# Kernel tuning notes

Hardware: AMD Instinct MI355X
Metric: run time of the kernel (lower is better)

The kernel has to match this reference:

```python
import jax, jax.numpy as jnp
import numpy as np
from jax import lax

REP_THR = 0.6
BORDER = 10


def setup_inputs() -> dict:
    key = jax.random.key(0)
    # repeatability heatmap in [0, 1), NCHW
    repeatability = jax.random.uniform(key, (16, 1, 1536, 1536), dtype=jnp.float32)
    return {"repeatability": repeatability}


def _local_max(x):
    # 3x3 stride-1 max pool with padding=1 (torch pads with -inf for maxpool)
    return lax.reduce_window(
        x, -jnp.inf, lax.max,
        window_dimensions=(1, 1, 3, 3),
        window_strides=(1, 1, 1, 1),
        padding=((0, 0), (0, 0), (1, 1), (1, 1)),
    )


def reference(repeatability):
    B, C, H, W = repeatability.shape
    maxima = (repeatability == _local_max(repeatability)) & (repeatability >= REP_THR)
    # border mask: zero out a 10-pixel frame
    border = jnp.zeros((H, W), dtype=bool).at[BORDER:-BORDER, BORDER:-BORDER].set(True)
    maxima = maxima & border  # broadcasts over (B, C)
    # nonzero().t()[2:4] -> row/col (y, x) coordinates of surviving maxima, shape [2, K]
    idx = jnp.nonzero(maxima)  # tuple (b, c, y, x); dynamic-shaped, eager only
    return jnp.stack(idx)[2:4]
```

## Files before the change

### kernel.cpp

```cpp
#include <hip/hip_runtime.h>

#define W 1536
#define H 1536
#define NB 16
#define NROWS (NB * H)
#define SH 32
#define NBLK1 (NROWS / SH)
#define BLOCK1 384
#define RING 8
#define CPR 24
#define NMASK (NROWS * CPR)
#define REP_THR 0.6f

__device__ __forceinline__ float max3f(float a, float b, float c) {
    return fmaxf(fmaxf(a, b), c);
}

__global__ __launch_bounds__(BLOCK1) void nms_pass1(const float* __restrict__ in,
                                                    unsigned long long* __restrict__ masks,
                                                    unsigned int* __restrict__ counts) {
    __shared__ float smem[RING * W];
    __shared__ unsigned wsum[BLOCK1 / 64];
    const int t = threadIdx.x;
    const int lane = t & 63;
    const int wv = t >> 6;
    const int blk = blockIdx.x;
    const int img = blk / 48;
    const int ytile = blk - img * 48;
    const int R0 = img * H + ytile * SH;
    const int rlo = R0 - 1;

    auto issue_step = [&](int s) {
        const int rel0 = 4 * s;
#pragma unroll
        for (int j = 0; j < 4; ++j) {
            int ir = rlo + rel0 + j;
            ir = ir < 0 ? 0 : (ir >= NROWS ? NROWS - 1 : ir);
            const float* g = in + (size_t)ir * W + 4 * t;
            float* l = smem + ((rel0 + j) & (RING - 1)) * W + (wv << 8);
            __builtin_amdgcn_global_load_lds(
                (const __attribute__((address_space(1))) unsigned int*)g,
                (__attribute__((address_space(3))) unsigned int*)l, 16, 0, 0);
        }
    };

    const int cl = (t == 0) ? 0 : (4 * t - 4);
    const int cr = (t == BLOCK1 - 1) ? 4 * t : (4 * t + 4);
    auto read_row = [&](int rel, float* r) {
        const float* base = smem + (rel & (RING - 1)) * W;
        float4 L = *(const float4*)(base + cl);
        float4 C = *(const float4*)(base + 4 * t);
        float4 R = *(const float4*)(base + cr);
        r[0] = L.w; r[1] = C.x; r[2] = C.y; r[3] = C.z; r[4] = C.w; r[5] = R.x;
    };

    unsigned colm = 0xFu;
    if (4 * t + 3 < 10) colm = 0u;
    else if (4 * t < 10) colm = 0xCu;
    if (4 * t > 1525) colm = 0u;
    else if (4 * t + 3 > 1525) colm &= 0x3u;

    issue_step(0);
    issue_step(1);

    float rA[6], rB[6], rC[6];
    unsigned cnt = 0;

#pragma unroll 1
    for (int s = 1; s <= SH / 4; ++s) {
        __syncthreads();
        if (s == 1) { read_row(0, rA); read_row(1, rB); }
        const int yb = ytile * SH + 4 * (s - 1);
#pragma unroll
        for (int r = 0; r < 4; ++r) {
            read_row(4 * (s - 1) + 2 + r, rC);
            const int y = yb + r;
            unsigned nib = 0u;
            if (y >= 10 && y < H - 10) {
                float cm0 = max3f(rA[0], rB[0], rC[0]);
                float cm1 = max3f(rA[1], rB[1], rC[1]);
                float cm2 = max3f(rA[2], rB[2], rC[2]);
                float cm3 = max3f(rA[3], rB[3], rC[3]);
                float cm4 = max3f(rA[4], rB[4], rC[4]);
                float cm5 = max3f(rA[5], rB[5], rC[5]);
                nib |= (rB[1] >= fmaxf(max3f(cm0, cm1, cm2), REP_THR)) ? 1u : 0u;
                nib |= (rB[2] >= fmaxf(max3f(cm1, cm2, cm3), REP_THR)) ? 2u : 0u;
                nib |= (rB[3] >= fmaxf(max3f(cm2, cm3, cm4), REP_THR)) ? 4u : 0u;
                nib |= (rB[4] >= fmaxf(max3f(cm3, cm4, cm5), REP_THR)) ? 8u : 0u;
                nib &= colm;
            }
#pragma unroll
            for (int k = 0; k < 6; ++k) { rA[k] = rB[k]; rB[k] = rC[k]; }
            cnt += __popc(nib);
            unsigned x = nib;
            x |= __shfl_down(x, 1, 64) << 4;
            x |= __shfl_down(x, 2, 64) << 8;
            x |= __shfl_down(x, 4, 64) << 16;
            unsigned hi = __shfl_down(x, 8, 64);
            if ((lane & 15) == 0) {
                unsigned long long m64 = (unsigned long long)x | ((unsigned long long)hi << 32);
                masks[(size_t)(img * H + y) * CPR + (t >> 4)] = m64;
            }
        }
        __syncthreads();
        if (s < SH / 4) issue_step(s + 1);
    }

#pragma unroll
    for (int o = 32; o > 0; o >>= 1) cnt += __shfl_down(cnt, o, 64);
    if (lane == 0) wsum[wv] = cnt;
    __syncthreads();
    if (t == 0) {
        unsigned sum = 0;
#pragma unroll
        for (int k = 0; k < BLOCK1 / 64; ++k) sum += wsum[k];
        counts[blk] = sum;
    }
}

__global__ __launch_bounds__(256) void nms_scan(const unsigned int* __restrict__ counts,
                                                unsigned int* __restrict__ offsets) {
    const int t = threadIdx.x;
    const int lane = t & 63, wv = t >> 6;
    unsigned v0 = counts[3 * t], v1 = counts[3 * t + 1], v2 = counts[3 * t + 2];
    unsigned sum = v0 + v1 + v2;
    unsigned incl = sum;
#pragma unroll
    for (int o = 1; o < 64; o <<= 1) {
        unsigned u = __shfl_up(incl, o, 64);
        if (lane >= o) incl += u;
    }
    __shared__ unsigned wtot[4];
    if (lane == 63) wtot[wv] = incl;
    __syncthreads();
    unsigned base = incl - sum;
#pragma unroll
    for (int k = 0; k < 4; ++k) base += (k < wv) ? wtot[k] : 0u;
    offsets[3 * t] = base;
    offsets[3 * t + 1] = base + v0;
    offsets[3 * t + 2] = base + v0 + v1;
}

__global__ __launch_bounds__(256) void nms_pass3(const unsigned long long* __restrict__ masks,
                                                 const unsigned int* __restrict__ offsets,
                                                 int* __restrict__ out, unsigned int K) {
    const int t = threadIdx.x, lane = t & 63, wv = t >> 6;
    const int blk = blockIdx.x;
    unsigned long long m[3];
    unsigned cnt = 0;
#pragma unroll
    for (int k = 0; k < 3; ++k) {
        m[k] = masks[(size_t)blk * (SH * CPR) + 3 * t + k];
        cnt += (unsigned)__popcll(m[k]);
    }
    unsigned incl = cnt;
#pragma unroll
    for (int o = 1; o < 64; o <<= 1) {
        unsigned u = __shfl_up(incl, o, 64);
        if (lane >= o) incl += u;
    }
    __shared__ unsigned wtot[4];
    if (lane == 63) wtot[wv] = incl;
    __syncthreads();
    unsigned wbase = 0;
#pragma unroll
    for (int k = 0; k < 4; ++k) wbase += (k < wv) ? wtot[k] : 0u;
    unsigned pos = offsets[blk] + wbase + (incl - cnt);
    const int ybase = (blk % 48) * SH;
#pragma unroll
    for (int k = 0; k < 3; ++k) {
        unsigned long long mm = m[k];
        if (mm) {
            const int q = 3 * t + k;
            const int y = ybase + q / CPR;
            const int x0 = (q % CPR) * 64;
            while (mm) {
                int j = __builtin_ctzll(mm);
                mm &= mm - 1ull;
                if (pos < K) { out[pos] = y; out[K + pos] = x0 + j; }
                ++pos;
            }
        }
    }
}

extern "C" void kernel_launch(void* const* d_in, const int* in_sizes, int n_in,
                              void* d_out, int out_size, void* d_ws, size_t ws_size,
                              hipStream_t stream) {
    const float* in = (const float*)d_in[0];
    int* out = (int*)d_out;
    unsigned long long* masks = (unsigned long long*)d_ws;
    unsigned int* counts = (unsigned int*)((char*)d_ws + (size_t)NMASK * 8);
    unsigned int* offsets = counts + NBLK1;
    const unsigned K = (unsigned)(out_size / 2);

    nms_pass1<<<NBLK1, BLOCK1, 0, stream>>>(in, masks, counts);
    nms_scan<<<1, 256, 0, stream>>>(counts, offsets);
    nms_pass3<<<NBLK1, 256, 0, stream>>>(masks, offsets, out, K);
}
```

Measured before the change: 267.2 us.

## Replace LDS ring staging with direct register loads and separable max

Drops the global_load_lds ring buffer and barriers in pass1. Each thread instead loads two overlapping unaligned float4s per row straight into registers, computes the horizontal 3-max once per row, and reuses it across the vertical window. The row tile is halved to 16 so there are twice as many blocks, and the scan and compaction kernels are resized to match. The aim is to remove LDS traffic and sync stalls, at the cost of unaligned and partly redundant global loads and more, shorter blocks.

```diff
diff --git a/kernel.cpp b/kernel.cpp
--- a/kernel.cpp
+++ b/kernel.cpp
@@ -4,10 +4,9 @@
 #define H 1536
 #define NB 16
 #define NROWS (NB * H)
-#define SH 32
+#define SH 16
 #define NBLK1 (NROWS / SH)
 #define BLOCK1 384
-#define RING 8
 #define CPR 24
 #define NMASK (NROWS * CPR)
 #define REP_THR 0.6f
@@ -16,105 +15,97 @@
     return fmaxf(fmaxf(a, b), c);
 }
 
+__device__ __forceinline__ float4 ld4u(const float* p) {
+    float4 r;
+    __builtin_memcpy(&r, p, 16);
+    return r;
+}
+
 __global__ __launch_bounds__(BLOCK1) void nms_pass1(const float* __restrict__ in,
                                                     unsigned long long* __restrict__ masks,
                                                     unsigned int* __restrict__ counts) {
-    __shared__ float smem[RING * W];
-    __shared__ unsigned wsum[BLOCK1 / 64];
     const int t = threadIdx.x;
     const int lane = t & 63;
     const int wv = t >> 6;
     const int blk = blockIdx.x;
-    const int img = blk / 48;
-    const int ytile = blk - img * 48;
-    const int R0 = img * H + ytile * SH;
-    const int rlo = R0 - 1;
+    const int r0 = blk * SH;
+    const int ytile = blk % (H / SH);
 
-    auto issue_step = [&](int s) {
-        const int rel0 = 4 * s;
-#pragma unroll
-        for (int j = 0; j < 4; ++j) {
-            int ir = rlo + rel0 + j;
-            ir = ir < 0 ? 0 : (ir >= NROWS ? NROWS - 1 : ir);
-            const float* g = in + (size_t)ir * W + 4 * t;
-            float* l = smem + ((rel0 + j) & (RING - 1)) * W + (wv << 8);
-            __builtin_amdgcn_global_load_lds(
-                (const __attribute__((address_space(1))) unsigned int*)g,
-                (__attribute__((address_space(3))) unsigned int*)l, 16, 0, 0);
-        }
+    const int ca = (t == 0) ? 0 : 4 * t - 1;
+    const int cb = (t == BLOCK1 - 1) ? 4 * t : 4 * t + 1;
+
+    unsigned colm = 0xFu;
+    if (t <= 1) colm = 0u;
+    else if (t == 2) colm = 0xCu;
+    if (t >= 382) colm = 0u;
+    else if (t == 381) colm = 0x3u;
+
+    auto rowp = [&](int i) {
+        int ir = r0 - 1 + i;
+        ir = ir < 0 ? 0 : (ir >= NROWS ? NROWS - 1 : ir);
+        return in + (size_t)ir * W;
     };
 
-    const int cl = (t == 0) ? 0 : (4 * t - 4);
-    const int cr = (t == BLOCK1 - 1) ? 4 * t : (4 * t + 4);
-    auto read_row = [&](int rel, float* r) {
-        const float* base = smem + (rel & (RING - 1)) * W;
-        float4 L = *(const float4*)(base + cl);
-        float4 C = *(const float4*)(base + 4 * t);
-        float4 R = *(const float4*)(base + cr);
-        r[0] = L.w; r[1] = C.x; r[2] = C.y; r[3] = C.z; r[4] = C.w; r[5] = R.x;
-    };
+    float4 va0 = ld4u(rowp(0) + ca), vb0 = ld4u(rowp(0) + cb);
+    float4 va1 = ld4u(rowp(1) + ca), vb1 = ld4u(rowp(1) + cb);
+    float4 vaN = ld4u(rowp(2) + ca), vbN = ld4u(rowp(2) + cb);
 
-    unsigned colm = 0xFu;
-    if (4 * t + 3 < 10) colm = 0u;
-    else if (4 * t < 10) colm = 0xCu;
-    if (4 * t > 1525) colm = 0u;
-    else if (4 * t + 3 > 1525) colm &= 0x3u;
+    float4 hA, hB, ctrB;
+    hA.x = max3f(va0.x, va0.y, va0.z);
+    hA.y = max3f(va0.y, va0.z, va0.w);
+    hA.z = max3f(vb0.x, vb0.y, vb0.z);
+    hA.w = max3f(vb0.y, vb0.z, vb0.w);
+    hB.x = max3f(va1.x, va1.y, va1.z);
+    hB.y = max3f(va1.y, va1.z, va1.w);
+    hB.z = max3f(vb1.x, vb1.y, vb1.z);
+    hB.w = max3f(vb1.y, vb1.z, vb1.w);
+    ctrB.x = va1.y; ctrB.y = va1.z; ctrB.z = va1.w; ctrB.w = vb1.z;
 
-    issue_step(0);
-    issue_step(1);
+    unsigned cnt = 0;
+#pragma unroll
+    for (int i = 2; i <= SH + 1; ++i) {
+        float4 va = vaN, vb = vbN;
+        vaN = ld4u(rowp(i + 1) + ca);
+        vbN = ld4u(rowp(i + 1) + cb);
+        float4 hC;
+        hC.x = max3f(va.x, va.y, va.z);
+        hC.y = max3f(va.y, va.z, va.w);
+        hC.z = max3f(vb.x, vb.y, vb.z);
+        hC.w = max3f(vb.y, vb.z, vb.w);
 
-    float rA[6], rB[6], rC[6];
-    unsigned cnt = 0;
-
-#pragma unroll 1
-    for (int s = 1; s <= SH / 4; ++s) {
-        __syncthreads();
-        if (s == 1) { read_row(0, rA); read_row(1, rB); }
-        const int yb = ytile * SH + 4 * (s - 1);
-#pragma unroll
-        for (int r = 0; r < 4; ++r) {
-            read_row(4 * (s - 1) + 2 + r, rC);
-            const int y = yb + r;
-            unsigned nib = 0u;
-            if (y >= 10 && y < H - 10) {
-                float cm0 = max3f(rA[0], rB[0], rC[0]);
-                float cm1 = max3f(rA[1], rB[1], rC[1]);
-                float cm2 = max3f(rA[2], rB[2], rC[2]);
-                float cm3 = max3f(rA[3], rB[3], rC[3]);
-                float cm4 = max3f(rA[4], rB[4], rC[4]);
-                float cm5 = max3f(rA[5], rB[5], rC[5]);
-                nib |= (rB[1] >= fmaxf(max3f(cm0, cm1, cm2), REP_THR)) ? 1u : 0u;
-                nib |= (rB[2] >= fmaxf(max3f(cm1, cm2, cm3), REP_THR)) ? 2u : 0u;
-                nib |= (rB[3] >= fmaxf(max3f(cm2, cm3, cm4), REP_THR)) ? 4u : 0u;
-                nib |= (rB[4] >= fmaxf(max3f(cm3, cm4, cm5), REP_THR)) ? 8u : 0u;
-                nib &= colm;
-            }
-#pragma unroll
-            for (int k = 0; k < 6; ++k) { rA[k] = rB[k]; rB[k] = rC[k]; }
-            cnt += __popc(nib);
-            unsigned x = nib;
-            x |= __shfl_down(x, 1, 64) << 4;
-            x |= __shfl_down(x, 2, 64) << 8;
-            x |= __shfl_down(x, 4, 64) << 16;
-            unsigned hi = __shfl_down(x, 8, 64);
-            if ((lane & 15) == 0) {
-                unsigned long long m64 = (unsigned long long)x | ((unsigned long long)hi << 32);
-                masks[(size_t)(img * H + y) * CPR + (t >> 4)] = m64;
-            }
+        const int yloc = ytile * SH + (i - 2);
+        unsigned nib = 0u;
+        if (yloc >= 10 && yloc < H - 10) {
+            nib |= (ctrB.x >= fmaxf(max3f(hA.x, hB.x, hC.x), REP_THR)) ? 1u : 0u;
+            nib |= (ctrB.y >= fmaxf(max3f(hA.y, hB.y, hC.y), REP_THR)) ? 2u : 0u;
+            nib |= (ctrB.z >= fmaxf(max3f(hA.z, hB.z, hC.z), REP_THR)) ? 4u : 0u;
+            nib |= (ctrB.w >= fmaxf(max3f(hA.w, hB.w, hC.w), REP_THR)) ? 8u : 0u;
+            nib &= colm;
         }
-        __syncthreads();
-        if (s < SH / 4) issue_step(s + 1);
+        cnt += __popc(nib);
+        unsigned x = nib;
+        x |= __shfl_down(x, 1, 64) << 4;
+        x |= __shfl_down(x, 2, 64) << 8;
+        x |= __shfl_down(x, 4, 64) << 16;
+        unsigned hi = __shfl_down(x, 8, 64);
+        if ((lane & 15) == 0) {
+            unsigned long long m64 = (unsigned long long)x | ((unsigned long long)hi << 32);
+            masks[(size_t)(r0 + i - 2) * CPR + (t >> 4)] = m64;
+        }
+        hA = hB; hB = hC;
+        ctrB.x = va.y; ctrB.y = va.z; ctrB.z = va.w; ctrB.w = vb.z;
     }
 
 #pragma unroll
     for (int o = 32; o > 0; o >>= 1) cnt += __shfl_down(cnt, o, 64);
+    __shared__ unsigned wsum[BLOCK1 / 64];
     if (lane == 0) wsum[wv] = cnt;
     __syncthreads();
     if (t == 0) {
-        unsigned sum = 0;
+        unsigned s = 0;
 #pragma unroll
-        for (int k = 0; k < BLOCK1 / 64; ++k) sum += wsum[k];
-        counts[blk] = sum;
+        for (int k = 0; k < BLOCK1 / 64; ++k) s += wsum[k];
+        counts[blk] = s;
     }
 }
 
@@ -122,8 +113,10 @@
                                                 unsigned int* __restrict__ offsets) {
     const int t = threadIdx.x;
     const int lane = t & 63, wv = t >> 6;
-    unsigned v0 = counts[3 * t], v1 = counts[3 * t + 1], v2 = counts[3 * t + 2];
-    unsigned sum = v0 + v1 + v2;
+    unsigned v[6];
+    unsigned sum = 0;
+#pragma unroll
+    for (int k = 0; k < 6; ++k) { v[k] = counts[t * 6 + k]; sum += v[k]; }
     unsigned incl = sum;
 #pragma unroll
     for (int o = 1; o < 64; o <<= 1) {
@@ -136,50 +129,38 @@
     unsigned base = incl - sum;
 #pragma unroll
     for (int k = 0; k < 4; ++k) base += (k < wv) ? wtot[k] : 0u;
-    offsets[3 * t] = base;
-    offsets[3 * t + 1] = base + v0;
-    offsets[3 * t + 2] = base + v0 + v1;
+#pragma unroll
+    for (int k = 0; k < 6; ++k) { offsets[t * 6 + k] = base; base += v[k]; }
 }
 
-__global__ __launch_bounds__(256) void nms_pass3(const unsigned long long* __restrict__ masks,
-                                                 const unsigned int* __restrict__ offsets,
-                                                 int* __restrict__ out, unsigned int K) {
+__global__ __launch_bounds__(BLOCK1) void nms_pass3(const unsigned long long* __restrict__ masks,
+                                                    const unsigned int* __restrict__ offsets,
+                                                    int* __restrict__ out, unsigned int K) {
     const int t = threadIdx.x, lane = t & 63, wv = t >> 6;
     const int blk = blockIdx.x;
-    unsigned long long m[3];
-    unsigned cnt = 0;
-#pragma unroll
-    for (int k = 0; k < 3; ++k) {
-        m[k] = masks[(size_t)blk * (SH * CPR) + 3 * t + k];
-        cnt += (unsigned)__popcll(m[k]);
-    }
+    unsigned long long bits = masks[(size_t)blk * (SH * CPR) + t];
+    const unsigned cnt = (unsigned)__popcll(bits);
     unsigned incl = cnt;
 #pragma unroll
     for (int o = 1; o < 64; o <<= 1) {
         unsigned u = __shfl_up(incl, o, 64);
         if (lane >= o) incl += u;
     }
-    __shared__ unsigned wtot[4];
+    __shared__ unsigned wtot[BLOCK1 / 64];
     if (lane == 63) wtot[wv] = incl;
     __syncthreads();
     unsigned wbase = 0;
 #pragma unroll
-    for (int k = 0; k < 4; ++k) wbase += (k < wv) ? wtot[k] : 0u;
+    for (int k = 0; k < BLOCK1 / 64; ++k) wbase += (k < wv) ? wtot[k] : 0u;
     unsigned pos = offsets[blk] + wbase + (incl - cnt);
-    const int ybase = (blk % 48) * SH;
-#pragma unroll
-    for (int k = 0; k < 3; ++k) {
-        unsigned long long mm = m[k];
-        if (mm) {
-            const int q = 3 * t + k;
-            const int y = ybase + q / CPR;
-            const int x0 = (q % CPR) * 64;
-            while (mm) {
-                int j = __builtin_ctzll(mm);
-                mm &= mm - 1ull;
-                if (pos < K) { out[pos] = y; out[K + pos] = x0 + j; }
-                ++pos;
-            }
+    if (bits) {
+        const int y = (blk % (H / SH)) * SH + t / CPR;
+        const int x0 = (t % CPR) * 64;
+        while (bits) {
+            int j = __builtin_ctzll(bits);
+            bits &= bits - 1ull;
+            if (pos < K) { out[pos] = y; out[K + pos] = x0 + j; }
+            ++pos;
         }
     }
 }
@@ -196,5 +177,5 @@
 
     nms_pass1<<<NBLK1, BLOCK1, 0, stream>>>(in, masks, counts);
     nms_scan<<<1, 256, 0, stream>>>(counts, offsets);
-    nms_pass3<<<NBLK1, 256, 0, stream>>>(masks, offsets, out, K);
+    nms_pass3<<<NBLK1, BLOCK1, 0, stream>>>(masks, offsets, out, K);
 }
```

New measurement: 246.3 us. 1.08x faster.
